# Optimization experiments

Measured on AMD Instinct MI355X. Metric: run time of the kernel, lower is better.

## Reference

```python
import jax, jax.numpy as jnp
import numpy as np

MODES = 128
WIDTH = 128
L_SEG = 20
M_CHEB = 8


def _cft_mag(x):
    # x: [B, C, N] real. Faithful port of vectorized_batched_cft_decomposed
    # (L=20 segments, M=8 Chebyshev nodes), restricted to the first MODES
    # frequencies (the only ones consumed downstream). Returns mean-|CFT|
    # over channels: [B, MODES]. Output is detached in the original code.
    n = x.shape[-1]
    t = jnp.linspace(0.0, 1.0, n)
    freqs = jnp.arange(MODES, dtype=jnp.float32)  # rfftfreq(n, d=1/n)[:MODES]
    seg_len = 1.0 / L_SEG
    a = jnp.linspace(0.0, 1.0, L_SEG + 1)[:-1]  # [L] segment starts
    k = jnp.arange(M_CHEB, dtype=jnp.float32)
    nodes = -jnp.cos((2.0 * k + 1.0) * jnp.pi / (2.0 * M_CHEB))  # [M]
    T = jnp.cos(k[:, None] * jnp.arccos(nodes)[None, :])  # [M(k), M(node)]
    w_prime = freqs * (2.0 * jnp.pi * seg_len / 2.0)  # [F]
    exp_q = jnp.exp(-1j * nodes[:, None] * w_prime[None, :])  # [M, F]
    cheb_w = (T @ exp_q) * (seg_len / 2.0)  # [M, F] complex
    shift = jnp.exp(-1j * 2.0 * jnp.pi * freqs[None, :] * a[:, None])  # [L, F]
    W = shift[:, None, :] * cheb_w[None, :, :]  # [L, M, F]
    # quadrature sample points and linear interpolation from the grid t
    t_seg = a[:, None] + seg_len / 2.0 * (nodes[None, :] + 1.0)  # [L, M]
    right = jnp.minimum(jnp.searchsorted(t, t_seg.reshape(-1)), n - 1).reshape(L_SEG, M_CHEB)
    left = jnp.maximum(right - 1, 0)
    tl, tr = t[left], t[right]
    denom = jnp.where(tr - tl == 0.0, 1.0, tr - tl)
    w_r = (t_seg - tl) / denom
    w_l = 1.0 - w_r
    sig = w_l[None, None] * x[:, :, left] + w_r[None, None] * x[:, :, right]  # [B,C,L,M]
    spec = jnp.einsum('bclm,lmf->bcf', sig.astype(jnp.complex64), W)  # [B,C,F]
    spec = jax.lax.stop_gradient(spec)  # .detach() in the original
    return jnp.mean(jnp.abs(spec), axis=1)  # [B, MODES]


def _forward(x, fc0_W, fc0_b, gate_W, gate_b, wA_re, wA_im, wB_re, wB_im,
             conv_W, conv_b, fc1_W, fc1_b, fc2_W, fc2_b):
    B, N, _ = x.shape
    grid = jnp.broadcast_to(jnp.linspace(0.0, 1.0, N)[None, :, None], (B, N, 1))
    h = jnp.concatenate([x, grid], axis=-1) @ fc0_W.T + fc0_b  # [B,N,W]
    h = h.transpose(0, 2, 1)  # [B,W,N]
    n_f = N // 2 + 1
    for i in range(4):
        mag = _cft_mag(h)  # [B, MODES], detached
        gate = jax.nn.sigmoid(mag @ gate_W[i].T + gate_b[i])  # [B, W]
        # weights1 = gate*A + (1-gate)*B, then the original einsum
        # 'bix,bioy->box' sums weights over the mode axis y; fold that sum
        # into the (in,out) matrices first.
        wA = (wA_re[i] + 1j * wA_im[i]).sum(-1)  # [in, out]
        wB = (wB_re[i] + 1j * wB_im[i]).sum(-1)
        Wg = gate[:, None, :] * wA[None] + (1.0 - gate[:, None, :]) * wB[None]  # [B,in,out]
        h_ft = jnp.fft.rfft(h)  # [B,W,n_f]
        out_modes = jnp.einsum('bif,bio->bof', h_ft[:, :, :MODES], Wg)
        out_ft = jnp.zeros((B, WIDTH, n_f), jnp.complex64).at[:, :, :MODES].set(out_modes)
        x1 = jnp.fft.irfft(out_ft, n=N)  # [B,W,N]
        x2 = jnp.einsum('bcn,oc->bon', h, conv_W[i]) + conv_b[i][None, :, None]
        h = x1 + x2
        if i < 3:
            h = jax.nn.gelu(h, approximate=False)
    h = h.transpose(0, 2, 1)  # [B,N,W]
    h = jax.nn.gelu(h @ fc1_W.T + fc1_b, approximate=False)
    return h @ fc2_W.T + fc2_b  # [B,N,1]


def setup_inputs() -> dict:
    key = jax.random.key(0)
    ks = jax.random.split(key, 16)
    B, N = 64, 4096
    scale = 1.0 / (WIDTH * WIDTH)
    d = {}
    d['x'] = jax.random.normal(ks[0], (B, N, 1), jnp.float32)
    d['fc0_W'] = jax.random.normal(ks[1], (WIDTH, 2), jnp.float32) * 0.1
    d['fc0_b'] = jnp.zeros((WIDTH,), jnp.float32)
    d['gate_W'] = jax.random.normal(ks[2], (4, WIDTH, MODES), jnp.float32) * 0.05
    d['gate_b'] = jnp.zeros((4, WIDTH), jnp.float32)
    d['wA_re'] = jax.random.uniform(ks[3], (4, WIDTH, WIDTH, MODES), jnp.float32) * scale
    d['wA_im'] = jax.random.uniform(ks[4], (4, WIDTH, WIDTH, MODES), jnp.float32) * scale
    d['wB_re'] = jax.random.uniform(ks[5], (4, WIDTH, WIDTH, MODES), jnp.float32) * scale
    d['wB_im'] = jax.random.uniform(ks[6], (4, WIDTH, WIDTH, MODES), jnp.float32) * scale
    d['conv_W'] = jax.random.normal(ks[7], (4, WIDTH, WIDTH), jnp.float32) * 0.05
    d['conv_b'] = jnp.zeros((4, WIDTH), jnp.float32)
    d['fc1_W'] = jax.random.normal(ks[8], (128, WIDTH), jnp.float32) * 0.05
    d['fc1_b'] = jnp.zeros((128,), jnp.float32)
    d['fc2_W'] = jax.random.normal(ks[9], (1, 128), jnp.float32) * 0.05
    d['fc2_b'] = jnp.zeros((1,), jnp.float32)
    return d


def reference(x, fc0_W, fc0_b, gate_W, gate_b, wA_re, wA_im, wB_re, wB_im,
              conv_W, conv_b, fc1_W, fc1_b, fc2_W, fc2_b):
    return _forward(x, fc0_W, fc0_b, gate_W, gate_b, wA_re, wA_im, wB_re, wB_im,
                    conv_W, conv_b, fc1_W, fc1_b, fc2_W, fc2_b)
```

## Files before the change

### kernel.cpp

```cpp
#include <hip/hip_runtime.h>
#include <math.h>

#define B_SZ 64
#define WID 128
#define NPT 4096
#define MODES 128
#define LSEG 20
#define MCH 8
#define LM 160

typedef _Float16 half8 __attribute__((ext_vector_type(8)));
typedef float f32x4 __attribute__((ext_vector_type(4)));

#define LO_SCALE 2048.0f
#define LO_INV   (1.0f/2048.0f)

static constexpr size_t BY_F    = 0;
static constexpr size_t BY_wsum = BY_F + 16777216;
static constexpr size_t BY_Wcre = BY_wsum + 1048576;
static constexpr size_t BY_Wcim = BY_Wcre + 81920;
static constexpr size_t BY_wl   = BY_Wcim + 81920;
static constexpr size_t BY_wr   = BY_wl + 1024;
static constexpr size_t BY_li   = BY_wr + 1024;
static constexpr size_t BY_magp = BY_li + 1024;
static constexpr size_t BY_gate = BY_magp + 524288;
static constexpr size_t BY_hh   = BY_gate + 32768;
static constexpr size_t BY_hl   = BY_hh + 67108864;
static constexpr size_t BY_Tfh  = BY_hl + 67108864;
static constexpr size_t BY_Tfl  = BY_Tfh + 2097152;
static constexpr size_t BY_Tih  = BY_Tfl + 2097152;
static constexpr size_t BY_Til  = BY_Tih + 2097152;
static constexpr size_t BY_Xh   = BY_Til + 2097152;
static constexpr size_t BY_Xl   = BY_Xh + 4194304;
static constexpr size_t BY_cWh  = BY_Xl + 4194304;
static constexpr size_t BY_cWl  = BY_cWh + 131072;
static constexpr size_t BY_f1h  = BY_cWl + 131072;
static constexpr size_t BY_f1l  = BY_f1h + 32768;
static constexpr size_t BY_end  = BY_f1l + 32768;

__device__ __forceinline__ float gelu_f(float x){
    return 0.5f*x*(1.0f+erff(x*0.70710678118654752f));
}
__device__ __forceinline__ void split_f16(float v, _Float16& hi, _Float16& lo){
    hi = (_Float16)v;
    lo = (_Float16)((v - (float)hi)*LO_SCALE);
}

__global__ void k_tables(_Float16* __restrict__ Tffh, _Float16* __restrict__ Tffl,
                         _Float16* __restrict__ Tifh, _Float16* __restrict__ Tifl){
    int idx = blockIdx.x*256 + threadIdx.x;
    int n = idx >> 8, k2 = idx & 255;
    int f = k2 >> 1;
    int m = (n*f) & 4095;
    double th = (double)m * (3.14159265358979323846/2048.0);
    double s, c; sincos(th, &s, &c);
    float vf = (k2&1) ? (float)(-s) : (float)c;
    {
        _Float16 h1,l1; split_f16(vf, h1, l1);
        int ct = k2>>4, ck = n>>5;
        int lane = (((n>>3)&3)<<4) | (k2&15);
        int j = n & 7;
        size_t off = (((size_t)(ct*128 + ck))<<9) + lane*8 + j;
        Tffh[off] = h1; Tffl[off] = l1;
    }
    float vi;
    if (k2 == 0)      vi = 1.0f;
    else if (k2 == 1) vi = 0.0f;
    else              vi = vf;
    {
        _Float16 h2,l2; split_f16(vi, h2, l2);
        int nt = n>>4, ck2 = k2>>5;
        int lane = (((k2>>3)&3)<<4) | (n&15);
        int j = k2 & 7;
        size_t off = (((size_t)(nt*8 + ck2))<<9) + lane*8 + j;
        Tifh[off] = h2; Tifl[off] = l2;
    }
}

__global__ void k_cft_tables(float* __restrict__ Wre, float* __restrict__ Wim,
                             float* __restrict__ wl, float* __restrict__ wr,
                             int* __restrict__ li){
    int idx = blockIdx.x*128 + threadIdx.x;
    if (idx >= LM*MODES) return;
    int lm = idx >> 7;  int f = idx & 127;
    int l = lm / MCH, m = lm % MCH;
    const double PI = 3.14159265358979323846;
    double nodes[8], Tm[8];
    #pragma unroll
    for (int j=0;j<8;j++){
        nodes[j] = -cos((2.0*j+1.0)*PI/16.0);
        Tm[j] = cos((double)m * acos(nodes[j]));
    }
    double wp = (double)f * PI * 0.05;
    double cwre=0.0, cwim=0.0;
    #pragma unroll
    for (int j=0;j<8;j++){
        double sj, cj; sincos(nodes[j]*wp, &sj, &cj);
        cwre += Tm[j]*cj;
        cwim -= Tm[j]*sj;
    }
    cwre *= 0.025; cwim *= 0.025;
    int r = (f*l) % 20;
    double sa = 2.0*PI*(double)r/20.0;
    double shre = cos(sa), shim = -sin(sa);
    Wre[lm*128+f] = (float)(shre*cwre - shim*cwim);
    Wim[lm*128+f] = (float)(shre*cwim + shim*cwre);
    if (f == 0){
        double v = (double)l/20.0 + 0.025*(nodes[m]+1.0);
        int rr = (int)ceil(v*4095.0);
        if (rr > 4095) rr = 4095;
        if (rr < 1) rr = 1;
        int le = rr-1;
        double tl = (double)le/4095.0, tr = (double)rr/4095.0;
        double wrv = (v - tl)/(tr - tl);
        li[lm] = le;
        wl[lm] = (float)(1.0 - wrv);
        wr[lm] = (float)wrv;
    }
}

__global__ void k_wsum(const float* __restrict__ wAre, const float* __restrict__ wAim,
                       const float* __restrict__ wBre, const float* __restrict__ wBim,
                       float* __restrict__ out){
    int row  = blockIdx.x*4 + (threadIdx.x>>6);
    int lane = threadIdx.x & 63;
    const float* src = (blockIdx.y==0)?wAre:(blockIdx.y==1)?wAim:(blockIdx.y==2)?wBre:wBim;
    float v = src[(size_t)row*128 + lane] + src[(size_t)row*128 + 64 + lane];
    #pragma unroll
    for (int o=32;o>0;o>>=1) v += __shfl_down(v, o);
    if (lane==0) out[(size_t)blockIdx.y*65536 + row] = v;
}

__global__ void k_wsplit(const float* __restrict__ convW, const float* __restrict__ fc1W,
                         _Float16* __restrict__ cWh, _Float16* __restrict__ cWl,
                         _Float16* __restrict__ f1h, _Float16* __restrict__ f1l){
    int idx = blockIdx.x*256 + threadIdx.x;
    if (idx < 65536){
        _Float16 hi,lo; split_f16(convW[idx], hi, lo);
        cWh[idx]=hi; cWl[idx]=lo;
    } else {
        int j = idx - 65536;
        _Float16 hi,lo; split_f16(fc1W[j], hi, lo);
        f1h[j]=hi; f1l[j]=lo;
    }
}

__global__ void k_h0(const float* __restrict__ x, const float* __restrict__ w0,
                     const float* __restrict__ b0,
                     _Float16* __restrict__ hh, _Float16* __restrict__ hl){
    int idx = blockIdx.x*256 + threadIdx.x;
    int n8 = idx & 511;
    int w  = (idx >> 9) & 127;
    int b  = idx >> 16;
    int n0 = n8*8;
    float w00 = w0[w*2], w01 = w0[w*2+1], bb = b0[w];
    const float* xr = &x[((size_t)b<<12) + n0];
    float4 x0 = *reinterpret_cast<const float4*>(xr);
    float4 x1 = *reinterpret_cast<const float4*>(xr+4);
    float xv[8]={x0.x,x0.y,x0.z,x0.w,x1.x,x1.y,x1.z,x1.w};
    half8 vh, vl;
    #pragma unroll
    for (int q=0;q<8;q++){
        float g = (float)(n0+q) * (1.0f/4095.0f);
        float v = xv[q]*w00 + g*w01 + bb;
        _Float16 hi,lo; split_f16(v,hi,lo);
        vh[q]=hi; vl[q]=lo;
    }
    size_t o = ((size_t)(b*128+w))*4096 + n0;
    *reinterpret_cast<half8*>(&hh[o]) = vh;
    *reinterpret_cast<half8*>(&hl[o]) = vl;
}

__global__ void k_cft(const _Float16* __restrict__ hh, const _Float16* __restrict__ hl,
                      const float* __restrict__ Wre, const float* __restrict__ Wim,
                      const float* __restrict__ wl, const float* __restrict__ wr,
                      const int* __restrict__ li, float* __restrict__ magp){
    int b = blockIdx.x, cg = blockIdx.y;
    int f = threadIdx.x;
    __shared__ float sig[LM];
    __shared__ float swl[LM], swr[LM];
    __shared__ int   sli[LM];
    for (int s=f; s<LM; s+=128){ swl[s]=wl[s]; swr[s]=wr[s]; sli[s]=li[s]; }
    __syncthreads();
    float acc = 0.f;
    for (int cc=0; cc<8; cc++){
        int c = cg*8 + cc;
        const _Float16* rh = hh + ((size_t)(b*128+c))*4096;
        const _Float16* rl = hl + ((size_t)(b*128+c))*4096;
        for (int s=f; s<LM; s+=128){
            int le = sli[s];
            float v0 = (float)rh[le]   + (float)rl[le]*LO_INV;
            float v1 = (float)rh[le+1] + (float)rl[le+1]*LO_INV;
            sig[s] = swl[s]*v0 + swr[s]*v1;
        }
        __syncthreads();
        float re=0.f, im=0.f;
        #pragma unroll 8
        for (int s=0;s<LM;s++){
            float sv = sig[s];
            re = fmaf(sv, Wre[s*128+f], re);
            im = fmaf(sv, Wim[s*128+f], im);
        }
        acc += sqrtf(re*re+im*im);
        __syncthreads();
    }
    magp[(b*16+cg)*128 + f] = acc;
}

__global__ void k_gate(const float* __restrict__ magp, const float* __restrict__ gW,
                       const float* __restrict__ gB, float* __restrict__ gate, int layer){
    int b = blockIdx.x, w = threadIdx.x;
    __shared__ float ms[128];
    float s = 0.f;
    #pragma unroll
    for (int g=0; g<16; g++) s += magp[(b*16+g)*128 + w];
    ms[w] = s * (1.0f/128.0f);
    __syncthreads();
    const float* gwr = gW + ((size_t)layer*128 + w)*128;
    float a = gB[layer*128 + w];
    #pragma unroll 8
    for (int fq=0; fq<128; fq++) a = fmaf(ms[fq], gwr[fq], a);
    gate[b*128+w] = 1.0f/(1.0f+expf(-a));
}

__global__ __launch_bounds__(256) void k_fdft(
        const _Float16* __restrict__ hh, const _Float16* __restrict__ hl,
        const _Float16* __restrict__ Tffh, const _Float16* __restrict__ Tffl,
        float* __restrict__ Fp){
    __shared__ _Float16 Ah[2][64][40], Al[2][64][40];
    int id = blockIdx.x;
    int swz = (id & 7)*64 + (id >> 3);
    int rg = swz & 127, cg = (swz >> 7) & 1, ks = swz >> 8;
    int row0 = rg*64, col0 = cg*128, kbase = ks*2048;
    int tid = threadIdx.x, lane = tid & 63, w = tid >> 6;
    int wr = (w>>1)*32, wc = (w&1)*64;
    int l15 = lane & 15, l4 = lane >> 4;
    f32x4 acc[2][4] = {}; f32x4 acc2[2][4] = {};
    int srow = tid >> 2, sseg = tid & 3;
    const _Float16* pa_h = hh + (size_t)(row0+srow)*4096 + kbase + sseg*8;
    const _Float16* pa_l = hl + (size_t)(row0+srow)*4096 + kbase + sseg*8;
    int ct0 = (col0 + wc) >> 4;
    int ckb = ks*64;
    const _Float16* pfh = Tffh + (size_t)lane*8;
    const _Float16* pfl = Tffl + (size_t)lane*8;
    half8 a0h,a0l,a1h,a1l;
    half8 bf0[8], bf1[8];
#define LOADA(xh,xl,ck) do{ \
    xh = *reinterpret_cast<const half8*>(pa_h + (size_t)(ck)*32); \
    xl = *reinterpret_cast<const half8*>(pa_l + (size_t)(ck)*32); }while(0)
#define WRITEA(xh,xl,buf) do{ \
    *reinterpret_cast<half8*>(&Ah[buf][srow][sseg*8]) = xh; \
    *reinterpret_cast<half8*>(&Al[buf][srow][sseg*8]) = xl; }while(0)
#define LOADB(dst,ck) do{ \
    _Pragma("unroll") for (int j=0;j<4;j++){ \
        dst[j]   = *reinterpret_cast<const half8*>(pfh + (((size_t)(ct0+j)*128 + ckb + (ck))<<9)); \
        dst[4+j] = *reinterpret_cast<const half8*>(pfl + (((size_t)(ct0+j)*128 + ckb + (ck))<<9)); } }while(0)
#define MMF(buf,BF) do{ \
    _Pragma("unroll") for (int i=0;i<2;i++){ \
        half8 fah = *reinterpret_cast<const half8*>(&Ah[buf][wr + i*16 + l15][l4*8]); \
        half8 fal = *reinterpret_cast<const half8*>(&Al[buf][wr + i*16 + l15][l4*8]); \
        _Pragma("unroll") for (int j=0;j<4;j++){ \
            acc[i][j]  = __builtin_amdgcn_mfma_f32_16x16x32_f16(fah, BF[j],   acc[i][j], 0,0,0); \
            acc2[i][j] = __builtin_amdgcn_mfma_f32_16x16x32_f16(fah, BF[4+j], acc2[i][j],0,0,0); \
            acc2[i][j] = __builtin_amdgcn_mfma_f32_16x16x32_f16(fal, BF[j],   acc2[i][j],0,0,0); } } }while(0)
    LOADA(a0h,a0l,0); WRITEA(a0h,a0l,0);
    LOADA(a0h,a0l,1);
    LOADA(a1h,a1l,2);
    LOADB(bf0,0); LOADB(bf1,1);
    __syncthreads();
    for (int tt=0; tt<32; ++tt){
        int t = tt*2;
        MMF(0,bf0);
        WRITEA(a0h,a0l,1);
        if (t+2 < 64) LOADB(bf0, t+2);
        if (t+3 < 64) LOADA(a0h,a0l, t+3);
        __syncthreads();
        MMF(1,bf1);
        if (t+2 < 64) WRITEA(a1h,a1l,0);
        if (t+3 < 64) LOADB(bf1, t+3);
        if (t+4 < 64) LOADA(a1h,a1l, t+4);
        __syncthreads();
    }
#undef LOADA
#undef WRITEA
#undef LOADB
#undef MMF
    float* Fo = Fp + (size_t)ks*2097152;
    #pragma unroll
    for (int i=0;i<2;i++)
        #pragma unroll
        for (int j=0;j<4;j++)
            #pragma unroll
            for (int r=0;r<4;r++){
                int row = row0 + wr + i*16 + l4*4 + r;
                int col = col0 + wc + j*16 + l15;
                Fo[(size_t)row*256 + col] = acc[i][j][r] + acc2[i][j][r]*LO_INV;
            }
}

__global__ __launch_bounds__(256) void k_modemix(const float* __restrict__ Fp,
        const float* __restrict__ wsum, const float* __restrict__ gate,
        _Float16* __restrict__ Xh, _Float16* __restrict__ Xl, int layer){
    int b = blockIdx.x, og = blockIdx.y;
    __shared__ float Fs[16][256];
    __shared__ float Wa_re[128][8], Wa_im[128][8], Wb_re[128][8], Wb_im[128][8];
    int tid = threadIdx.x;
    for (int e=tid; e<1024; e+=256){
        int i = e>>3, oo = e&7;
        size_t base = ((size_t)layer*128 + i)*128 + og*8 + oo;
        Wa_re[i][oo] = wsum[0*65536 + base];
        Wa_im[i][oo] = wsum[1*65536 + base];
        Wb_re[i][oo] = wsum[2*65536 + base];
        Wb_im[i][oo] = wsum[3*65536 + base];
    }
    int f = tid & 127, half = tid >> 7;
    float pre[4]={},pim[4]={},qre[4]={},qim[4]={};
    for (int i0=0;i0<128;i0+=16){
        for (int e=tid; e<4096; e+=256){
            int ii = e >> 8, k2 = e & 255;
            size_t idx = ((size_t)(b*128 + i0+ii))*256 + k2;
            Fs[ii][k2] = Fp[idx] + Fp[idx + 2097152];
        }
        __syncthreads();
        #pragma unroll
        for (int ii=0; ii<16; ii++){
            float fre = Fs[ii][2*f], fim = Fs[ii][2*f+1];
            int i = i0+ii;
            #pragma unroll
            for (int q=0;q<4;q++){
                int oo = half*4+q;
                float are=Wa_re[i][oo], aim=Wa_im[i][oo];
                float bre=Wb_re[i][oo], bim=Wb_im[i][oo];
                pre[q] = fmaf(fre, are, fmaf(-fim, aim, pre[q]));
                pim[q] = fmaf(fre, aim, fmaf( fim, are, pim[q]));
                qre[q] = fmaf(fre, bre, fmaf(-fim, bim, qre[q]));
                qim[q] = fmaf(fre, bim, fmaf( fim, bre, qim[q]));
            }
        }
        __syncthreads();
    }
    #pragma unroll
    for (int q=0;q<4;q++){
        int o = og*8 + half*4 + q;
        float g = gate[b*128+o];
        float xre = g*pre[q] + (1.f-g)*qre[q];
        float xim = g*pim[q] + (1.f-g)*qim[q];
        float s = (f==0) ? (1.0f/4096.0f) : (2.0f/4096.0f);
        xre *= s; xim *= s;
        if (f==0) xim = 0.f;
        size_t base = ((size_t)(b*128+o))*256 + 2*f;
        _Float16 h1,l1; split_f16(xre,h1,l1); Xh[base]=h1;   Xl[base]=l1;
        _Float16 h2,l2; split_f16(xim,h2,l2); Xh[base+1]=h2; Xl[base+1]=l2;
    }
}

__global__ __launch_bounds__(256) void k_flayer(
    const _Float16* __restrict__ Xh, const _Float16* __restrict__ Xl,
    const _Float16* __restrict__ Tifh, const _Float16* __restrict__ Tifl,
    const _Float16* __restrict__ cWh, const _Float16* __restrict__ cWl,
    const float* __restrict__ convB,
    _Float16* __restrict__ hh, _Float16* __restrict__ hl,
    int layer, int applyGelu){
    __shared__ _Float16 As_h[2][128][40], As_l[2][128][40];
    __shared__ _Float16 Bs_h[2][64][40],  Bs_l[2][64][40];
    int n0 = blockIdx.x*64;
    int b  = blockIdx.y;
    int tid = threadIdx.x, lane = tid & 63, w = tid >> 6;
    int l15 = lane & 15, l4 = lane >> 4;
    int o0 = w*32;
    int aro = tid >> 2, asl = tid & 3;
    int ctc = tid >> 3, ctn = tid & 7;
    int ocp = ((tid >> 6) ^ (tid & 3));
    const _Float16* cA_h = cWh + (size_t)layer*16384 + (size_t)aro*128 + asl*8;
    const _Float16* cA_l = cWl + (size_t)layer*16384 + (size_t)aro*128 + asl*8;
    const _Float16* xA_h = Xh + ((size_t)(b*128 + aro))*256 + asl*8;
    const _Float16* xA_l = Xl + ((size_t)(b*128 + aro))*256 + asl*8;
    const _Float16* hB_h = hh + ((size_t)(b*128 + ctc))*4096 + n0 + ctn*8;
    const _Float16* hB_l = hl + ((size_t)(b*128 + ctc))*4096 + n0 + ctn*8;
    int nt0 = n0 >> 4;
    const _Float16* pTh = Tifh + (size_t)lane*8;
    const _Float16* pTl = Tifl + (size_t)lane*8;
    f32x4 acc[2][4] = {}; f32x4 acc2[2][4] = {};
    half8 rA[6], rB[6];
    half8 bf0[8], bf1[8];
#define LOADR(r,ck) do{ \
    if ((ck) < 4){ size_t kk = (size_t)(ck)*32; \
        r[0] = *reinterpret_cast<const half8*>(cA_h + kk); \
        r[1] = *reinterpret_cast<const half8*>(cA_l + kk); \
        r[2] = *reinterpret_cast<const half8*>(cA_h + 64*128 + kk); \
        r[3] = *reinterpret_cast<const half8*>(cA_l + 64*128 + kk); \
        r[4] = *reinterpret_cast<const half8*>(hB_h + (size_t)(ck)*32*4096); \
        r[5] = *reinterpret_cast<const half8*>(hB_l + (size_t)(ck)*32*4096); \
    } else { size_t kk = (size_t)((ck)-4)*32; \
        r[0] = *reinterpret_cast<const half8*>(xA_h + kk); \
        r[1] = *reinterpret_cast<const half8*>(xA_l + kk); \
        r[2] = *reinterpret_cast<const half8*>(xA_h + 64*256 + kk); \
        r[3] = *reinterpret_cast<const half8*>(xA_l + 64*256 + kk); } }while(0)
#define WRITER(r,buf,ck) do{ \
    *reinterpret_cast<half8*>(&As_h[buf][aro][asl*8])    = r[0]; \
    *reinterpret_cast<half8*>(&As_l[buf][aro][asl*8])    = r[1]; \
    *reinterpret_cast<half8*>(&As_h[buf][aro+64][asl*8]) = r[2]; \
    *reinterpret_cast<half8*>(&As_l[buf][aro+64][asl*8]) = r[3]; \
    if ((ck) < 4){ \
        _Pragma("unroll") for (int j2=0;j2<8;j2++){ \
            int n1 = ctn*8 + j2; \
            Bs_h[buf][n1][ocp*8 + (ctc&7)] = r[4][j2]; \
            Bs_l[buf][n1][ocp*8 + (ctc&7)] = r[5][j2]; } } }while(0)
#define LOADBF(dst,ckp) do{ \
    _Pragma("unroll") for (int j=0;j<4;j++){ \
        dst[j]   = *reinterpret_cast<const half8*>(pTh + (((size_t)((nt0+j)*8 + (ckp)))<<9)); \
        dst[4+j] = *reinterpret_cast<const half8*>(pTl + (((size_t)((nt0+j)*8 + (ckp)))<<9)); } }while(0)
#define MML(buf,ck,BF) do{ \
    half8 bh[4], bl[4]; \
    if ((ck) < 4){ \
        _Pragma("unroll") for (int j=0;j<4;j++){ \
            int n = j*16 + l15; int sl = (l4 ^ ((n>>3)&3)); \
            bh[j] = *reinterpret_cast<const half8*>(&Bs_h[buf][n][sl*8]); \
            bl[j] = *reinterpret_cast<const half8*>(&Bs_l[buf][n][sl*8]); } \
    } else { \
        _Pragma("unroll") for (int j=0;j<4;j++){ bh[j] = BF[j]; bl[j] = BF[4+j]; } } \
    _Pragma("unroll") for (int i=0;i<2;i++){ \
        half8 ah = *reinterpret_cast<const half8*>(&As_h[buf][o0+i*16+l15][l4*8]); \
        half8 al = *reinterpret_cast<const half8*>(&As_l[buf][o0+i*16+l15][l4*8]); \
        _Pragma("unroll") for (int j=0;j<4;j++){ \
            acc[i][j]  = __builtin_amdgcn_mfma_f32_16x16x32_f16(ah, bh[j], acc[i][j], 0,0,0); \
            acc2[i][j] = __builtin_amdgcn_mfma_f32_16x16x32_f16(ah, bl[j], acc2[i][j],0,0,0); \
            acc2[i][j] = __builtin_amdgcn_mfma_f32_16x16x32_f16(al, bh[j], acc2[i][j],0,0,0); } } }while(0)
    LOADR(rA, 0);
    WRITER(rA, 0, 0);
    LOADR(rA, 1);
    LOADR(rB, 2);
    __syncthreads();
    #pragma unroll
    for (int tt=0; tt<6; ++tt){
        const int t = 2*tt;
        MML(0, t, bf0);
        WRITER(rA, 1, t+1);
        if (t+2 >= 4 && t+2 < 12) LOADBF(bf0, t+2-4);
        if (t+3 < 12) LOADR(rA, t+3);
        __syncthreads();
        MML(1, t+1, bf1);
        if (t+2 < 12) WRITER(rB, 0, t+2);
        if (t+3 >= 4 && t+3 < 12) LOADBF(bf1, t+3-4);
        if (t+4 < 12) LOADR(rB, t+4);
        __syncthreads();
    }
#undef LOADR
#undef WRITER
#undef LOADBF
#undef MML
    #pragma unroll
    for (int i=0;i<2;i++)
        #pragma unroll
        for (int j=0;j<4;j++)
            #pragma unroll
            for (int r=0;r<4;r++){
                int o = o0 + i*16 + l4*4 + r;
                int n = n0 + j*16 + l15;
                float v = acc[i][j][r] + acc2[i][j][r]*LO_INV + convB[layer*128+o];
                if (applyGelu) v = gelu_f(v);
                _Float16 hi,lo; split_f16(v,hi,lo);
                size_t oi = ((size_t)(b*128+o))*4096 + n;
                hh[oi] = hi; hl[oi] = lo;
            }
}

__global__ __launch_bounds__(256) void k_head(
        const _Float16* __restrict__ hh, const _Float16* __restrict__ hl,
        const _Float16* __restrict__ f1h, const _Float16* __restrict__ f1l,
        const float* __restrict__ fc1b,
        const float* __restrict__ fc2W, const float* __restrict__ fc2b,
        float* __restrict__ out){
    __shared__ _Float16 Bch[64][136], Bcl[64][136];
    __shared__ _Float16 Ash[128][40], Asl[128][40];
    __shared__ float red[16][64];
    int n0 = blockIdx.x*64;
    int b  = blockIdx.y;
    int tid = threadIdx.x, lane = tid & 63, w = tid >> 6;
    int l15 = lane & 15, l4 = lane >> 4;
    int j0 = w*32;
    {
        int c = tid & 127, nh = tid >> 7;
        const _Float16* rh = hh + ((size_t)(b*128+c))*4096 + n0 + nh*32;
        const _Float16* rl = hl + ((size_t)(b*128+c))*4096 + n0 + nh*32;
        #pragma unroll
        for (int j=0;j<4;j++){
            half8 vhv = *reinterpret_cast<const half8*>(rh + j*8);
            half8 vlv = *reinterpret_cast<const half8*>(rl + j*8);
            #pragma unroll
            for (int q=0;q<8;q++){
                int n = nh*32 + j*8 + q;
                Bch[n][c] = vhv[q];
                Bcl[n][c] = vlv[q];
            }
        }
    }
    __syncthreads();
    int so2 = tid >> 2, sseg = tid & 3;
    f32x4 acc[2][4] = {}; f32x4 acc2[2][4] = {};
    for (int k0=0;k0<128;k0+=32){
        #pragma unroll
        for (int p=0;p<2;p++){
            int o = p*64 + so2;
            *reinterpret_cast<half8*>(&Ash[o][sseg*8]) =
                *reinterpret_cast<const half8*>(&f1h[(size_t)o*128 + k0 + sseg*8]);
            *reinterpret_cast<half8*>(&Asl[o][sseg*8]) =
                *reinterpret_cast<const half8*>(&f1l[(size_t)o*128 + k0 + sseg*8]);
        }
        __syncthreads();
        half8 ah[2],al[2],bh[4],bl[4];
        #pragma unroll
        for (int i=0;i<2;i++){
            ah[i] = *reinterpret_cast<const half8*>(&Ash[j0+i*16+l15][l4*8]);
            al[i] = *reinterpret_cast<const half8*>(&Asl[j0+i*16+l15][l4*8]);
        }
        #pragma unroll
        for (int j=0;j<4;j++){
            bh[j] = *reinterpret_cast<const half8*>(&Bch[j*16+l15][k0+l4*8]);
            bl[j] = *reinterpret_cast<const half8*>(&Bcl[j*16+l15][k0+l4*8]);
        }
        #pragma unroll
        for (int i=0;i<2;i++)
            #pragma unroll
            for (int j=0;j<4;j++){
                acc[i][j]  = __builtin_amdgcn_mfma_f32_16x16x32_f16(ah[i], bh[j], acc[i][j], 0,0,0);
                acc2[i][j] = __builtin_amdgcn_mfma_f32_16x16x32_f16(ah[i], bl[j], acc2[i][j],0,0,0);
                acc2[i][j] = __builtin_amdgcn_mfma_f32_16x16x32_f16(al[i], bh[j], acc2[i][j],0,0,0);
            }
        __syncthreads();
    }
    float part[4];
    #pragma unroll
    for (int j=0;j<4;j++) part[j] = 0.f;
    #pragma unroll
    for (int i=0;i<2;i++){
        #pragma unroll
        for (int r=0;r<4;r++){
            int jj = j0 + i*16 + l4*4 + r;
            float b1 = fc1b[jj];
            float w2 = fc2W[jj];
            #pragma unroll
            for (int j=0;j<4;j++){
                float v = acc[i][j][r] + acc2[i][j][r]*LO_INV + b1;
                part[j] = fmaf(w2, gelu_f(v), part[j]);
            }
        }
    }
    #pragma unroll
    for (int j=0;j<4;j++) red[w*4+l4][j*16+l15] = part[j];
    __syncthreads();
    if (tid < 64){
        float s = fc2b[0];
        #pragma unroll
        for (int r=0;r<16;r++) s += red[r][tid];
        out[((size_t)b<<12) + n0 + tid] = s;
    }
}

extern "C" void kernel_launch(void* const* d_in, const int* in_sizes, int n_in,
                              void* d_out, int out_size, void* d_ws, size_t ws_size,
                              hipStream_t stream) {
    const float* x     = (const float*)d_in[0];
    const float* fc0W  = (const float*)d_in[1];
    const float* fc0b  = (const float*)d_in[2];
    const float* gateW = (const float*)d_in[3];
    const float* gateB = (const float*)d_in[4];
    const float* wAre  = (const float*)d_in[5];
    const float* wAim  = (const float*)d_in[6];
    const float* wBre  = (const float*)d_in[7];
    const float* wBim  = (const float*)d_in[8];
    const float* convW = (const float*)d_in[9];
    const float* convB = (const float*)d_in[10];
    const float* fc1W  = (const float*)d_in[11];
    const float* fc1b  = (const float*)d_in[12];
    const float* fc2W  = (const float*)d_in[13];
    const float* fc2b  = (const float*)d_in[14];
    float* out = (float*)d_out;
    char*  wsb = (char*)d_ws;

    float* Fp   = (float*)(wsb + BY_F);
    float* wsum = (float*)(wsb + BY_wsum);
    float* Wcre = (float*)(wsb + BY_Wcre);
    float* Wcim = (float*)(wsb + BY_Wcim);
    float* wl   = (float*)(wsb + BY_wl);
    float* wr   = (float*)(wsb + BY_wr);
    int*   li   = (int*)(wsb + BY_li);
    float* magp = (float*)(wsb + BY_magp);
    float* gate = (float*)(wsb + BY_gate);
    _Float16* hh   = (_Float16*)(wsb + BY_hh);
    _Float16* hl   = (_Float16*)(wsb + BY_hl);
    _Float16* Tffh = (_Float16*)(wsb + BY_Tfh);
    _Float16* Tffl = (_Float16*)(wsb + BY_Tfl);
    _Float16* Tifh = (_Float16*)(wsb + BY_Tih);
    _Float16* Tifl = (_Float16*)(wsb + BY_Til);
    _Float16* Xh   = (_Float16*)(wsb + BY_Xh);
    _Float16* Xl   = (_Float16*)(wsb + BY_Xl);
    _Float16* cWh  = (_Float16*)(wsb + BY_cWh);
    _Float16* cWl  = (_Float16*)(wsb + BY_cWl);
    _Float16* f1h  = (_Float16*)(wsb + BY_f1h);
    _Float16* f1l  = (_Float16*)(wsb + BY_f1l);

    k_tables<<<4096, 256, 0, stream>>>(Tffh, Tffl, Tifh, Tifl);
    k_cft_tables<<<160, 128, 0, stream>>>(Wcre, Wcim, wl, wr, li);
    k_wsum<<<dim3(16384,4), 256, 0, stream>>>(wAre, wAim, wBre, wBim, wsum);
    k_wsplit<<<320, 256, 0, stream>>>(convW, fc1W, cWh, cWl, f1h, f1l);
    k_h0<<<16384, 256, 0, stream>>>(x, fc0W, fc0b, hh, hl);

    for (int layer=0; layer<4; layer++){
        k_cft<<<dim3(64,16), 128, 0, stream>>>(hh, hl, Wcre, Wcim, wl, wr, li, magp);
        k_gate<<<64, 128, 0, stream>>>(magp, gateW, gateB, gate, layer);
        k_fdft<<<512, 256, 0, stream>>>(hh, hl, Tffh, Tffl, Fp);
        k_modemix<<<dim3(64,16), 256, 0, stream>>>(Fp, wsum, gate, Xh, Xl, layer);
        k_flayer<<<dim3(64,64), 256, 0, stream>>>(Xh, Xl, Tifh, Tifl, cWh, cWl, convB,
                                                  hh, hl, layer, layer<3 ? 1:0);
    }
    k_head<<<dim3(64,64), 256, 0, stream>>>(hh, hl, f1h, f1l, fc1b, fc2W, fc2b, out);
    (void)in_sizes; (void)n_in; (void)out_size; (void)ws_size;
}
```

Before: 1.338 ms.

## Recast spectral mode mixing as split-f16 MFMA GEMM plus separate gate blend

After: 1.239 ms. -7.4%, faster.

```diff
diff --git a/kernel.cpp b/kernel.cpp
--- a/kernel.cpp
+++ b/kernel.cpp
@@ -11,12 +11,14 @@
 
 typedef _Float16 half8 __attribute__((ext_vector_type(8)));
 typedef float f32x4 __attribute__((ext_vector_type(4)));
+typedef float float2v __attribute__((ext_vector_type(2)));
 
 #define LO_SCALE 2048.0f
 #define LO_INV   (1.0f/2048.0f)
 
 static constexpr size_t BY_F    = 0;
-static constexpr size_t BY_wsum = BY_F + 16777216;
+static constexpr size_t BY_P    = BY_F + 16777216;
+static constexpr size_t BY_wsum = BY_P + 16777216;
 static constexpr size_t BY_Wcre = BY_wsum + 1048576;
 static constexpr size_t BY_Wcim = BY_Wcre + 81920;
 static constexpr size_t BY_wl   = BY_Wcim + 81920;
@@ -36,7 +38,11 @@
 static constexpr size_t BY_cWl  = BY_cWh + 131072;
 static constexpr size_t BY_f1h  = BY_cWl + 131072;
 static constexpr size_t BY_f1l  = BY_f1h + 32768;
-static constexpr size_t BY_end  = BY_f1l + 32768;
+static constexpr size_t BY_Bph  = BY_f1l + 32768;
+static constexpr size_t BY_Bpl  = BY_Bph + 1048576;
+static constexpr size_t BY_ct   = BY_Bpl + 1048576;
+static constexpr size_t BY_st   = BY_ct + 16384;
+static constexpr size_t BY_end  = BY_st + 16384;
 
 __device__ __forceinline__ float gelu_f(float x){
     return 0.5f*x*(1.0f+erff(x*0.70710678118654752f));
@@ -46,21 +52,28 @@
     lo = (_Float16)((v - (float)hi)*LO_SCALE);
 }
 
-__global__ void k_tables(_Float16* __restrict__ Tffh, _Float16* __restrict__ Tffl,
+__global__ void k_trig(float* __restrict__ ct, float* __restrict__ st){
+    int m = blockIdx.x*256 + threadIdx.x;
+    double th = (double)m * (3.14159265358979323846/2048.0);
+    double s, c; sincos(th, &s, &c);
+    ct[m] = (float)c; st[m] = (float)s;
+}
+
+__global__ void k_tables(const float* __restrict__ ct, const float* __restrict__ st,
+                         _Float16* __restrict__ Tffh, _Float16* __restrict__ Tffl,
                          _Float16* __restrict__ Tifh, _Float16* __restrict__ Tifl){
     int idx = blockIdx.x*256 + threadIdx.x;
     int n = idx >> 8, k2 = idx & 255;
     int f = k2 >> 1;
     int m = (n*f) & 4095;
-    double th = (double)m * (3.14159265358979323846/2048.0);
-    double s, c; sincos(th, &s, &c);
-    float vf = (k2&1) ? (float)(-s) : (float)c;
+    float cv = ct[m], sv = st[m];
+    float vf = (k2&1) ? -sv : cv;
     {
         _Float16 h1,l1; split_f16(vf, h1, l1);
-        int ct = k2>>4, ck = n>>5;
+        int ctile = k2>>4, ck = n>>5;
         int lane = (((n>>3)&3)<<4) | (k2&15);
         int j = n & 7;
-        size_t off = (((size_t)(ct*128 + ck))<<9) + lane*8 + j;
+        size_t off = (((size_t)(ctile*128 + ck))<<9) + lane*8 + j;
         Tffh[off] = h1; Tffl[off] = l1;
     }
     float vi;
@@ -129,6 +142,27 @@
     #pragma unroll
     for (int o=32;o>0;o>>=1) v += __shfl_down(v, o);
     if (lane==0) out[(size_t)blockIdx.y*65536 + row] = v;
+}
+
+__global__ void k_bprime(const float* __restrict__ wsum,
+                         _Float16* __restrict__ Bph, _Float16* __restrict__ Bpl){
+    int idx = blockIdx.x*256 + threadIdx.x;
+    int layer = idx >> 17;
+    int e = idx & 131071;
+    int kp = e >> 9, n = e & 511;
+    int i = kp >> 1, c = kp & 1;
+    int quad = n >> 7, o = n & 127;
+    size_t base = (size_t)layer*16384 + (size_t)i*128 + o;
+    float v;
+    if (quad==0)      v = c ? -wsum[65536 + base]   : wsum[base];
+    else if (quad==1) v = c ?  wsum[base]           : wsum[65536 + base];
+    else if (quad==2) v = c ? -wsum[3*65536 + base] : wsum[2*65536 + base];
+    else              v = c ?  wsum[2*65536 + base] : wsum[3*65536 + base];
+    _Float16 hi,lo; split_f16(v,hi,lo);
+    int ck = kp >> 5, kloc = kp & 31, nt = n >> 4;
+    size_t off = (size_t)layer*131072 + (((size_t)(nt*8 + ck))<<9)
+               + (size_t)((((kloc>>3)&3)<<4) | (n&15))*8 + (kloc&7);
+    Bph[off]=hi; Bpl[off]=lo;
 }
 
 __global__ void k_wsplit(const float* __restrict__ convW, const float* __restrict__ fc1W,
@@ -298,60 +332,116 @@
             }
 }
 
-__global__ __launch_bounds__(256) void k_modemix(const float* __restrict__ Fp,
-        const float* __restrict__ wsum, const float* __restrict__ gate,
-        _Float16* __restrict__ Xh, _Float16* __restrict__ Xl, int layer){
+__global__ __launch_bounds__(256) void k_pmix(
+        const float* __restrict__ Fp,
+        const _Float16* __restrict__ Bph, const _Float16* __restrict__ Bpl,
+        float* __restrict__ P, int layer){
+    __shared__ _Float16 Ash[64][40], Asl[64][40];
+    int mt = blockIdx.x;
+    int nb = blockIdx.y;
+    int b  = mt >> 1;
+    int f0 = (mt & 1) * 64;
+    int tid = threadIdx.x, lane = tid & 63, w = tid >> 6;
+    int wr = (w>>1)*32, wn = (w&1)*64;
+    int l15 = lane & 15, l4 = lane >> 4;
+    int sf = tid & 63, sig = tid >> 6;
+    f32x4 acc[2][4] = {}; f32x4 acc2[2][4] = {};
+    int nt0 = (nb*128 + wn) >> 4;
+    const _Float16* pBh = Bph + (size_t)layer*131072 + (size_t)lane*8;
+    const _Float16* pBl = Bpl + (size_t)layer*131072 + (size_t)lane*8;
+    for (int ck=0; ck<8; ++ck){
+        #pragma unroll
+        for (int q=0;q<4;q++){
+            int i = ck*16 + sig*4 + q;
+            size_t idx = ((size_t)(b*128 + i))*256 + 2*(f0+sf);
+            float2v v0 = *reinterpret_cast<const float2v*>(&Fp[idx]);
+            float2v v1 = *reinterpret_cast<const float2v*>(&Fp[idx + 2097152]);
+            float re = v0.x + v1.x, im = v0.y + v1.y;
+            int kloc = 2*(sig*4+q);
+            _Float16 h0,l0,h1,l1;
+            split_f16(re,h0,l0); split_f16(im,h1,l1);
+            Ash[sf][kloc] = h0; Ash[sf][kloc+1] = h1;
+            Asl[sf][kloc] = l0; Asl[sf][kloc+1] = l1;
+        }
+        __syncthreads();
+        half8 bh[4], bl[4];
+        #pragma unroll
+        for (int j=0;j<4;j++){
+            size_t off = ((size_t)((nt0+j)*8 + ck)) << 9;
+            bh[j] = *reinterpret_cast<const half8*>(pBh + off);
+            bl[j] = *reinterpret_cast<const half8*>(pBl + off);
+        }
+        #pragma unroll
+        for (int i=0;i<2;i++){
+            half8 ah = *reinterpret_cast<const half8*>(&Ash[wr+i*16+l15][l4*8]);
+            half8 al = *reinterpret_cast<const half8*>(&Asl[wr+i*16+l15][l4*8]);
+            #pragma unroll
+            for (int j=0;j<4;j++){
+                acc[i][j]  = __builtin_amdgcn_mfma_f32_16x16x32_f16(ah, bh[j], acc[i][j], 0,0,0);
+                acc2[i][j] = __builtin_amdgcn_mfma_f32_16x16x32_f16(ah, bl[j], acc2[i][j],0,0,0);
+                acc2[i][j] = __builtin_amdgcn_mfma_f32_16x16x32_f16(al, bh[j], acc2[i][j],0,0,0);
+            }
+        }
+        __syncthreads();
+    }
+    int m0 = mt*64;
+    #pragma unroll
+    for (int i=0;i<2;i++)
+        #pragma unroll
+        for (int j=0;j<4;j++)
+            #pragma unroll
+            for (int r=0;r<4;r++){
+                int row = wr + i*16 + l4*4 + r;
+                int col = wn + j*16 + l15;
+                P[(size_t)(m0+row)*512 + nb*128 + col] = acc[i][j][r] + acc2[i][j][r]*LO_INV;
+            }
+}
+
+__global__ __launch_bounds__(256) void k_gmix(
+        const float* __restrict__ P, const float* __restrict__ gate,
+        _Float16* __restrict__ Xh, _Float16* __restrict__ Xl){
+    __shared__ float S[128][16][4];
     int b = blockIdx.x, og = blockIdx.y;
-    __shared__ float Fs[16][256];
-    __shared__ float Wa_re[128][8], Wa_im[128][8], Wb_re[128][8], Wb_im[128][8];
     int tid = threadIdx.x;
-    for (int e=tid; e<1024; e+=256){
-        int i = e>>3, oo = e&7;
-        size_t base = ((size_t)layer*128 + i)*128 + og*8 + oo;
-        Wa_re[i][oo] = wsum[0*65536 + base];
-        Wa_im[i][oo] = wsum[1*65536 + base];
-        Wb_re[i][oo] = wsum[2*65536 + base];
-        Wb_im[i][oo] = wsum[3*65536 + base];
-    }
-    int f = tid & 127, half = tid >> 7;
-    float pre[4]={},pim[4]={},qre[4]={},qim[4]={};
-    for (int i0=0;i0<128;i0+=16){
-        for (int e=tid; e<4096; e+=256){
-            int ii = e >> 8, k2 = e & 255;
-            size_t idx = ((size_t)(b*128 + i0+ii))*256 + k2;
-            Fs[ii][k2] = Fp[idx] + Fp[idx + 2097152];
-        }
-        __syncthreads();
-        #pragma unroll
-        for (int ii=0; ii<16; ii++){
-            float fre = Fs[ii][2*f], fim = Fs[ii][2*f+1];
-            int i = i0+ii;
+    {
+        int f = tid >> 1, seg = tid & 1;
+        #pragma unroll
+        for (int qq=0; qq<2; ++qq){
+            int quad = seg*2 + qq;
+            const float* src = &P[((size_t)(b*128+f))*512 + quad*128 + og*16];
             #pragma unroll
-            for (int q=0;q<4;q++){
-                int oo = half*4+q;
-                float are=Wa_re[i][oo], aim=Wa_im[i][oo];
-                float bre=Wb_re[i][oo], bim=Wb_im[i][oo];
-                pre[q] = fmaf(fre, are, fmaf(-fim, aim, pre[q]));
-                pim[q] = fmaf(fre, aim, fmaf( fim, are, pim[q]));
-                qre[q] = fmaf(fre, bre, fmaf(-fim, bim, qre[q]));
-                qim[q] = fmaf(fre, bim, fmaf( fim, bre, qim[q]));
+            for (int jj=0; jj<4; ++jj){
+                float4 v = *reinterpret_cast<const float4*>(src + jj*4);
+                S[f][jj*4+0][quad] = v.x;
+                S[f][jj*4+1][quad] = v.y;
+                S[f][jj*4+2][quad] = v.z;
+                S[f][jj*4+3][quad] = v.w;
             }
         }
-        __syncthreads();
-    }
-    #pragma unroll
-    for (int q=0;q<4;q++){
-        int o = og*8 + half*4 + q;
-        float g = gate[b*128+o];
-        float xre = g*pre[q] + (1.f-g)*qre[q];
-        float xim = g*pim[q] + (1.f-g)*qim[q];
+    }
+    __syncthreads();
+    int oo = tid & 15, fg = tid >> 4;
+    int o = og*16 + oo;
+    float g = gate[b*128 + o];
+    half8 xh0, xh1, xl0, xl1;
+    #pragma unroll
+    for (int ff=0; ff<8; ++ff){
+        int f = fg*8 + ff;
+        float pre = g*S[f][oo][0] + (1.f-g)*S[f][oo][2];
+        float pim = g*S[f][oo][1] + (1.f-g)*S[f][oo][3];
         float s = (f==0) ? (1.0f/4096.0f) : (2.0f/4096.0f);
-        xre *= s; xim *= s;
-        if (f==0) xim = 0.f;
-        size_t base = ((size_t)(b*128+o))*256 + 2*f;
-        _Float16 h1,l1; split_f16(xre,h1,l1); Xh[base]=h1;   Xl[base]=l1;
-        _Float16 h2,l2; split_f16(xim,h2,l2); Xh[base+1]=h2; Xl[base+1]=l2;
-    }
+        pre *= s; pim *= s;
+        if (f==0) pim = 0.f;
+        _Float16 h0,l0,h1,l1;
+        split_f16(pre,h0,l0); split_f16(pim,h1,l1);
+        if (ff<4){ xh0[2*ff]=h0; xh0[2*ff+1]=h1; xl0[2*ff]=l0; xl0[2*ff+1]=l1; }
+        else { xh1[2*(ff-4)]=h0; xh1[2*(ff-4)+1]=h1; xl1[2*(ff-4)]=l0; xl1[2*(ff-4)+1]=l1; }
+    }
+    size_t base = ((size_t)(b*128+o))*256 + fg*16;
+    *reinterpret_cast<half8*>(&Xh[base])   = xh0;
+    *reinterpret_cast<half8*>(&Xh[base+8]) = xh1;
+    *reinterpret_cast<half8*>(&Xl[base])   = xl0;
+    *reinterpret_cast<half8*>(&Xl[base+8]) = xl1;
 }
 
 __global__ __launch_bounds__(256) void k_flayer(
@@ -579,6 +669,7 @@
     char*  wsb = (char*)d_ws;
 
     float* Fp   = (float*)(wsb + BY_F);
+    float* P    = (float*)(wsb + BY_P);
     float* wsum = (float*)(wsb + BY_wsum);
     float* Wcre = (float*)(wsb + BY_Wcre);
     float* Wcim = (float*)(wsb + BY_Wcim);
@@ -599,10 +690,16 @@
     _Float16* cWl  = (_Float16*)(wsb + BY_cWl);
     _Float16* f1h  = (_Float16*)(wsb + BY_f1h);
     _Float16* f1l  = (_Float16*)(wsb + BY_f1l);
-
-    k_tables<<<4096, 256, 0, stream>>>(Tffh, Tffl, Tifh, Tifl);
+    _Float16* Bph  = (_Float16*)(wsb + BY_Bph);
+    _Float16* Bpl  = (_Float16*)(wsb + BY_Bpl);
+    float* ct   = (float*)(wsb + BY_ct);
+    float* st   = (float*)(wsb + BY_st);
+
+    k_trig<<<16, 256, 0, stream>>>(ct, st);
+    k_tables<<<4096, 256, 0, stream>>>(ct, st, Tffh, Tffl, Tifh, Tifl);
     k_cft_tables<<<160, 128, 0, stream>>>(Wcre, Wcim, wl, wr, li);
     k_wsum<<<dim3(16384,4), 256, 0, stream>>>(wAre, wAim, wBre, wBim, wsum);
+    k_bprime<<<2048, 256, 0, stream>>>(wsum, Bph, Bpl);
     k_wsplit<<<320, 256, 0, stream>>>(convW, fc1W, cWh, cWl, f1h, f1l);
     k_h0<<<16384, 256, 0, stream>>>(x, fc0W, fc0b, hh, hl);
 
@@ -610,7 +707,8 @@
         k_cft<<<dim3(64,16), 128, 0, stream>>>(hh, hl, Wcre, Wcim, wl, wr, li, magp);
         k_gate<<<64, 128, 0, stream>>>(magp, gateW, gateB, gate, layer);
         k_fdft<<<512, 256, 0, stream>>>(hh, hl, Tffh, Tffl, Fp);
-        k_modemix<<<dim3(64,16), 256, 0, stream>>>(Fp, wsum, gate, Xh, Xl, layer);
+        k_pmix<<<dim3(128,4), 256, 0, stream>>>(Fp, Bph, Bpl, P, layer);
+        k_gmix<<<dim3(64,8), 256, 0, stream>>>(P, gate, Xh, Xl);
         k_flayer<<<dim3(64,64), 256, 0, stream>>>(Xh, Xl, Tifh, Tifl, cWh, cWl, convB,
                                                   hh, hl, layer, layer<3 ? 1:0);
     }
```
